# Kernel tuning notes

Measured on AMD Instinct MI355X. Metric: run time of the kernel, lower is better.

Reference implementation:

```python
import jax, jax.numpy as jnp
import numpy as np

NUM_F, K, EMB, N_NODE = 50000, 32, 128, 100000


def setup_inputs() -> dict:
    key = jax.random.key(0)
    k1, k2, k3, k4, k5, k6 = jax.random.split(key, 6)
    stdv = 1.0 / np.sqrt(EMB)
    return {
        "adjacency_fi": jax.random.randint(k1, (NUM_F, K), 0, N_NODE, dtype=jnp.int64)
        if jax.config.jax_enable_x64 else jax.random.randint(k1, (NUM_F, K), 0, N_NODE, dtype=jnp.int32),
        "embedding_i": jax.random.normal(k2, (N_NODE, EMB), dtype=jnp.float32),
        "embedding_f_weight": jax.random.uniform(k3, (NUM_F, EMB), jnp.float32, -stdv, stdv),
        "u": jax.random.uniform(k4, (EMB, 1), jnp.float32, -stdv, stdv),
        "W_weight": jax.random.uniform(k5, (EMB, 2 * EMB), jnp.float32, -stdv, stdv),
        "W_bias": jax.random.uniform(k6, (EMB,), jnp.float32, -stdv, stdv),
    }


def reference(adjacency_fi, embedding_i, embedding_f_weight, u, W_weight, W_bias):
    # Gather neighbor embeddings: [F, K, E]
    neigh = embedding_i[adjacency_fi]
    # Rank-1 attention score with additive padding mask (index 0 = pad)
    mask = jnp.where(adjacency_fi != 0, 0.0, -10000.0).astype(neigh.dtype)  # [F, K]
    alpha = jnp.einsum("fke,eo->fk", neigh, u) + mask
    alpha = jax.nn.softmax(alpha, axis=-1)
    agg = jnp.einsum("fk,fke->fe", alpha, neigh)  # [F, E]  (dropout70: eval mode, identity)
    # Gated fusion: gate = sigmoid(Linear(cat([emb_f, agg])))
    cat = jnp.concatenate([embedding_f_weight, agg], axis=1)  # [F, 2E]
    gate = jax.nn.sigmoid(cat @ W_weight.T + W_bias)  # [F, E]
    new_emb = gate * embedding_f_weight + (1.0 - gate) * agg  # (dropout50: eval mode, identity)
    return new_emb
```

## Files before the change

### kernel.cpp

```cpp
#include <hip/hip_runtime.h>

#define F_TOTAL 50000
#define KNBR    32
#define EMB     128
#define FB      16
#define RPW     4
#define CHK     8

__global__ __launch_bounds__(256, 4)
void fused_gnn(const int*   __restrict__ adj,
               const float* __restrict__ embi,
               const float* __restrict__ embf,
               const float* __restrict__ u,
               const float* __restrict__ W,
               const float* __restrict__ bias,
               float*       __restrict__ out)
{
    __shared__ float catbuf[FB][2 * EMB];
    __shared__ float pbuf[FB][EMB];

    const int tid   = threadIdx.x;
    const int wave  = tid >> 6;
    const int lane  = tid & 63;
    const int fbase = blockIdx.x * FB;

    const float2 uv = *(const float2*)(u + 2 * lane);

    for (int i = 0; i < RPW; ++i) {
        const int r = wave * RPW + i;
        const int f = fbase + r;

        const int myidx = adj[f * KNBR + (lane & 31)];

        float m = -3.0e38f;
        float s = 0.0f;
        float2 acc = make_float2(0.f, 0.f);

#pragma unroll
        for (int c = 0; c < KNBR / CHK; ++c) {
            float2 nb[CHK];
#pragma unroll
            for (int j = 0; j < CHK; ++j) {
                const int ik = __shfl(myidx, c * CHK + j);
                nb[j] = *(const float2*)(embi + (size_t)ik * EMB + 2 * lane);
            }

            float v[CHK];
#pragma unroll
            for (int j = 0; j < CHK; ++j)
                v[j] = nb[j].x * uv.x + nb[j].y * uv.y;

#pragma unroll
            for (int bit = 4; bit >= 1; bit >>= 1) {
                const bool upper = (lane & bit) != 0;
#pragma unroll
                for (int j = 0; j < bit; ++j) {
                    const float send = upper ? v[j] : v[j + bit];
                    const float recv = __shfl_xor(send, bit);
                    v[j] = (upper ? v[j + bit] : v[j]) + recv;
                }
            }
            float alpha = v[0];
            alpha += __shfl_xor(alpha, 8);
            alpha += __shfl_xor(alpha, 16);
            alpha += __shfl_xor(alpha, 32);

            const int ikown = __shfl(myidx, c * CHK + (lane & 7));
            alpha += (ikown != 0) ? 0.0f : -10000.0f;

            float cm = alpha;
            cm = fmaxf(cm, __shfl_xor(cm, 1));
            cm = fmaxf(cm, __shfl_xor(cm, 2));
            cm = fmaxf(cm, __shfl_xor(cm, 4));

            const float mnew  = fmaxf(m, cm);
            const float scale = __expf(m - mnew);
            s *= scale;
            acc.x *= scale;
            acc.y *= scale;
            m = mnew;

            const float e = __expf(alpha - mnew);
            float se = e;
            se += __shfl_xor(se, 1);
            se += __shfl_xor(se, 2);
            se += __shfl_xor(se, 4);
            s += se;

#pragma unroll
            for (int j = 0; j < CHK; ++j) {
                const float w = __shfl(e, j);
                acc.x += w * nb[j].x;
                acc.y += w * nb[j].y;
            }
        }

        const float inv = 1.0f / s;
        acc.x *= inv;
        acc.y *= inv;

        const float2 ef = *(const float2*)(embf + (size_t)f * EMB + 2 * lane);
        *(float2*)&catbuf[r][2 * lane]       = ef;
        *(float2*)&catbuf[r][EMB + 2 * lane] = acc;
    }
    __syncthreads();

    const int p  = tid & 63;
    const int g  = tid >> 6;
    const int c0 = 2 * p, c1 = c0 + 1;
    const int jbase = g * 64;

    float acc0[FB], acc1[FB];
#pragma unroll
    for (int r = 0; r < FB; ++r) { acc0[r] = 0.f; acc1[r] = 0.f; }

    const float* W0 = W + (size_t)c0 * (2 * EMB) + jbase;
    const float* W1 = W + (size_t)c1 * (2 * EMB) + jbase;

#pragma unroll 4
    for (int j = 0; j < 64; j += 4) {
        const float4 w0 = *(const float4*)(W0 + j);
        const float4 w1 = *(const float4*)(W1 + j);
#pragma unroll
        for (int r = 0; r < FB; ++r) {
            const float4 cv = *(const float4*)&catbuf[r][jbase + j];
            acc0[r] += cv.x * w0.x + cv.y * w0.y + cv.z * w0.z + cv.w * w0.w;
            acc1[r] += cv.x * w1.x + cv.y * w1.y + cv.z * w1.z + cv.w * w1.w;
        }
    }

    if (g == 3) {
#pragma unroll
        for (int r = 0; r < FB; ++r) { pbuf[r][c0] = acc0[r]; pbuf[r][c1] = acc1[r]; }
    }
    __syncthreads();
    if (g == 2) {
#pragma unroll
        for (int r = 0; r < FB; ++r) { pbuf[r][c0] += acc0[r]; pbuf[r][c1] += acc1[r]; }
    }
    __syncthreads();
    if (g == 1) {
#pragma unroll
        for (int r = 0; r < FB; ++r) { pbuf[r][c0] += acc0[r]; pbuf[r][c1] += acc1[r]; }
    }
    __syncthreads();
    if (g == 0) {
        const float2 bv = *(const float2*)(bias + c0);
#pragma unroll
        for (int r = 0; r < FB; ++r) {
            const float t0 = acc0[r] + pbuf[r][c0] + bv.x;
            const float t1 = acc1[r] + pbuf[r][c1] + bv.y;
            const float g0 = 1.f / (1.f + __expf(-t0));
            const float g1 = 1.f / (1.f + __expf(-t1));
            const float e0 = catbuf[r][c0],       e1 = catbuf[r][c1];
            const float a0 = catbuf[r][EMB + c0], a1 = catbuf[r][EMB + c1];
            float2 o;
            o.x = g0 * e0 + (1.f - g0) * a0;
            o.y = g1 * e1 + (1.f - g1) * a1;
            *(float2*)(out + (size_t)(fbase + r) * EMB + c0) = o;
        }
    }
}

extern "C" void kernel_launch(void* const* d_in, const int* in_sizes, int n_in,
                              void* d_out, int out_size, void* d_ws, size_t ws_size,
                              hipStream_t stream) {
    const int*   adj  = (const int*)  d_in[0];
    const float* embi = (const float*)d_in[1];
    const float* embf = (const float*)d_in[2];
    const float* u    = (const float*)d_in[3];
    const float* W    = (const float*)d_in[4];
    const float* bias = (const float*)d_in[5];
    float* outp = (float*)d_out;

    fused_gnn<<<F_TOTAL / FB, 256, 0, stream>>>(adj, embi, embf, u, W, bias, outp);
}
```

Measured before the change: 324.2 us.

## Double-buffer neighbor gathers and drop online-max softmax rescaling

Neighbor embedding rows for the next chunk of 8 are loaded into a second register buffer while the current chunk is scored and accumulated. The aim is to overlap the random gather latency with compute. The online max/rescale softmax is replaced by a plain exp of the raw scores: padding is handled through a ballot bitmask, and the denominator is reduced once at the end. Broadcasts use readlane instead of shuffles. This raises register pressure and removes overflow protection, so it depends on the attention scores staying small. It also yields NaN if every neighbor is padding.

```diff
diff --git a/kernel.cpp b/kernel.cpp
--- a/kernel.cpp
+++ b/kernel.cpp
@@ -31,24 +31,37 @@
         const int f = fbase + r;
 
         const int myidx = adj[f * KNBR + (lane & 31)];
+        const unsigned long long nz = __ballot(myidx != 0);
 
-        float m = -3.0e38f;
-        float s = 0.0f;
+        const float2 ef = *(const float2*)(embf + (size_t)f * EMB + 2 * lane);
+
+        float2 nbA[CHK], nbB[CHK];
+#pragma unroll
+        for (int j = 0; j < CHK; ++j) {
+            const unsigned ik = (unsigned)__builtin_amdgcn_readlane(myidx, j);
+            nbA[j] = *(const float2*)(embi + (size_t)ik * EMB + 2 * lane);
+        }
+
         float2 acc = make_float2(0.f, 0.f);
+        float  se  = 0.f;
 
 #pragma unroll
         for (int c = 0; c < KNBR / CHK; ++c) {
-            float2 nb[CHK];
+            float2* cur = (c & 1) ? nbB : nbA;
+            float2* nxt = (c & 1) ? nbA : nbB;
+            if (c < KNBR / CHK - 1) {
 #pragma unroll
-            for (int j = 0; j < CHK; ++j) {
-                const int ik = __shfl(myidx, c * CHK + j);
-                nb[j] = *(const float2*)(embi + (size_t)ik * EMB + 2 * lane);
+                for (int j = 0; j < CHK; ++j) {
+                    const unsigned ik = (unsigned)__builtin_amdgcn_readlane(
+                        myidx, (c + 1) * CHK + j);
+                    nxt[j] = *(const float2*)(embi + (size_t)ik * EMB + 2 * lane);
+                }
             }
 
             float v[CHK];
 #pragma unroll
             for (int j = 0; j < CHK; ++j)
-                v[j] = nb[j].x * uv.x + nb[j].y * uv.y;
+                v[j] = cur[j].x * uv.x + cur[j].y * uv.y;
 
 #pragma unroll
             for (int bit = 4; bit >= 1; bit >>= 1) {
@@ -65,41 +78,27 @@
             alpha += __shfl_xor(alpha, 16);
             alpha += __shfl_xor(alpha, 32);
 
-            const int ikown = __shfl(myidx, c * CHK + (lane & 7));
-            alpha += (ikown != 0) ? 0.0f : -10000.0f;
-
-            float cm = alpha;
-            cm = fmaxf(cm, __shfl_xor(cm, 1));
-            cm = fmaxf(cm, __shfl_xor(cm, 2));
-            cm = fmaxf(cm, __shfl_xor(cm, 4));
-
-            const float mnew  = fmaxf(m, cm);
-            const float scale = __expf(m - mnew);
-            s *= scale;
-            acc.x *= scale;
-            acc.y *= scale;
-            m = mnew;
-
-            const float e = __expf(alpha - mnew);
-            float se = e;
-            se += __shfl_xor(se, 1);
-            se += __shfl_xor(se, 2);
-            se += __shfl_xor(se, 4);
-            s += se;
+            const int kg = c * CHK + (lane & 7);
+            const float e = ((nz >> kg) & 1ull) ? __expf(alpha) : 0.0f;
+            se += e;
 
 #pragma unroll
             for (int j = 0; j < CHK; ++j) {
-                const float w = __shfl(e, j);
-                acc.x += w * nb[j].x;
-                acc.y += w * nb[j].y;
+                const float w = __uint_as_float((unsigned)__builtin_amdgcn_readlane(
+                    (int)__float_as_uint(e), j));
+                acc.x = fmaf(w, cur[j].x, acc.x);
+                acc.y = fmaf(w, cur[j].y, acc.y);
             }
         }
 
-        const float inv = 1.0f / s;
+        float S = se;
+        S += __shfl_xor(S, 1);
+        S += __shfl_xor(S, 2);
+        S += __shfl_xor(S, 4);
+        const float inv = 1.0f / S;
         acc.x *= inv;
         acc.y *= inv;
 
-        const float2 ef = *(const float2*)(embf + (size_t)f * EMB + 2 * lane);
         *(float2*)&catbuf[r][2 * lane]       = ef;
         *(float2*)&catbuf[r][EMB + 2 * lane] = acc;
     }
```

Result: faster. 293.7 us (-9.4%).
